# Kernel tuning notes

Hardware: AMD Instinct MI355X
Metric: run time of the kernel (lower is better)

The kernel has to match this reference:

```python
import jax, jax.numpy as jnp
import numpy as np

D = 1024

def setup_inputs() -> dict:
    key = jax.random.key(0)
    ks = jax.random.split(key, 9)
    s = 1.0 / np.sqrt(D)
    x = jax.random.normal(ks[0], (8, 4096, D), dtype=jnp.float32)
    Wq = jax.random.uniform(ks[1], (D, D), jnp.float32, -s, s)
    bq = jax.random.uniform(ks[2], (D,), jnp.float32, -s, s)
    Wk = jax.random.uniform(ks[3], (D, D), jnp.float32, -s, s)
    bk = jax.random.uniform(ks[4], (D,), jnp.float32, -s, s)
    Wv = jax.random.uniform(ks[5], (D, D), jnp.float32, -s, s)
    bv = jax.random.uniform(ks[6], (D,), jnp.float32, -s, s)
    Wo = jax.random.uniform(ks[7], (D, D), jnp.float32, -s, s)
    bo = jax.random.uniform(ks[8], (D,), jnp.float32, -s, s)
    return {"x": x, "Wq": Wq, "bq": bq, "Wk": Wk, "bk": bk,
            "Wv": Wv, "bv": bv, "Wo": Wo, "bo": bo}

def reference(x, Wq, bq, Wk, bk, Wv, bv, Wo, bo):
    # Linear projections (torch Linear: x @ W.T + b)
    Q = x @ Wq.T + bq
    K = x @ Wk.T + bk
    V = x @ Wv.T + bv
    # elu+1 feature map (positive features)
    Q = jax.nn.elu(Q) + 1.0
    K = jax.nn.elu(K) + 1.0
    # KV outer-product accumulation over sequence: [b, d, e]
    KV = jnp.einsum('bnd,bne->bde', K, V)
    # normalizer Z: [b, n]
    Z = jnp.einsum('bnd,bd->bn', Q, K.sum(axis=1) + 1e-6)
    context = jnp.einsum('bnd,bde->bne', Q, KV) / Z[..., None]
    return context @ Wo.T + bo
```

## Files before the change

### kernel.cpp

```cpp
#include <hip/hip_runtime.h>
#include <stdint.h>

typedef unsigned short u16;
typedef __attribute__((ext_vector_type(8))) short short8;
typedef __attribute__((ext_vector_type(4))) float f32x4;

#define SEQ    4096
#define NB     8
#define DMODEL 1024
#define MTOT   (NB*SEQ)

static __device__ __forceinline__ float bf2f(u16 u){
  union { float f; uint32_t i; } v; v.i = ((uint32_t)u) << 16; return v.f;
}
static __device__ __forceinline__ u16 f2bf(float f){
  union { float f; uint32_t i; } v; v.f = f;
  uint32_t i = v.i + 0x7FFFu + ((v.i >> 16) & 1u);
  return (u16)(i >> 16);
}

static __device__ __forceinline__ void stage16(const void* g, void* l){
  __builtin_amdgcn_global_load_lds(
      (const __attribute__((address_space(1))) void*)g,
      (__attribute__((address_space(3))) void*)l,
      16, 0, 0);
}

__global__ void cvt_f32_bf16(const float* __restrict__ s, u16* __restrict__ d, int n){
  int i = (blockIdx.x * 256 + threadIdx.x) * 8;
  if (i >= n) return;
  float4 a = *(const float4*)(s + i);
  float4 b = *(const float4*)(s + i + 4);
  union { u16 h[8]; short8 v; } o;
  o.h[0]=f2bf(a.x); o.h[1]=f2bf(a.y); o.h[2]=f2bf(a.z); o.h[3]=f2bf(a.w);
  o.h[4]=f2bf(b.x); o.h[5]=f2bf(b.y); o.h[6]=f2bf(b.z); o.h[7]=f2bf(b.w);
  *(short8*)(d + i) = o.v;
}

__global__ __launch_bounds__(256)
void cvt_tr(const float* __restrict__ in, u16* __restrict__ outN,
            u16* __restrict__ outT, int R, int C)
{
  __shared__ float t[64][65];
  const int tid = threadIdx.x;
  const int ntc = C >> 6;
  const int tr = blockIdx.x / ntc, tc = blockIdx.x % ntc;
  const int r0 = tr << 6, c0 = tc << 6;
  const int lrow = tid >> 4, lc4 = (tid & 15) << 2;
  #pragma unroll
  for (int p = 0; p < 4; p++){
    float4 v = *(const float4*)(in + (size_t)(r0 + p*16 + lrow) * C + c0 + lc4);
    t[p*16 + lrow][lc4+0] = v.x; t[p*16 + lrow][lc4+1] = v.y;
    t[p*16 + lrow][lc4+2] = v.z; t[p*16 + lrow][lc4+3] = v.w;
  }
  __syncthreads();
  const int wrow = tid >> 3, wc8 = (tid & 7) << 3;
  if (outN){
    #pragma unroll
    for (int p = 0; p < 2; p++){
      int r = p*32 + wrow;
      union { u16 h[8]; short8 v; } o;
      #pragma unroll
      for (int j = 0; j < 8; j++) o.h[j] = f2bf(t[r][wc8 + j]);
      *(short8*)(outN + (size_t)(r0 + r) * C + c0 + wc8) = o.v;
    }
  }
  #pragma unroll
  for (int p = 0; p < 2; p++){
    int c = p*32 + wrow;
    union { u16 h[8]; short8 v; } o;
    #pragma unroll
    for (int j = 0; j < 8; j++) o.h[j] = f2bf(t[wc8 + j][c]);
    *(short8*)(outT + (size_t)(c0 + c) * R + r0 + wc8) = o.v;
  }
}

__global__ void bo2_kernel(const float* __restrict__ Wo, const float* __restrict__ bv,
                           const float* __restrict__ bo, float* __restrict__ bo2){
  int o = blockIdx.x * 4 + (threadIdx.x >> 6);
  int lane = threadIdx.x & 63;
  const float* row = Wo + (size_t)o * DMODEL;
  float s = 0.f;
  #pragma unroll
  for (int j = 0; j < 4; j++){
    float4 w = *(const float4*)(row + j*256 + lane*4);
    float4 b = *(const float4*)(bv  + j*256 + lane*4);
    s += w.x*b.x + w.y*b.y + w.z*b.z + w.w*b.w;
  }
  for (int off = 32; off; off >>= 1) s += __shfl_xor(s, off);
  if (lane == 0) bo2[o] = bo[o] + s;
}

__global__ void ksum_kernel(const u16* __restrict__ Kt, float* __restrict__ Ksum){
  int wid  = blockIdx.x * 4 + (threadIdx.x >> 6);
  int lane = threadIdx.x & 63;
  int d = wid & 1023, b = wid >> 10;
  const u16* row = Kt + (size_t)d * MTOT + (size_t)b * SEQ;
  float s = 0.f;
  #pragma unroll
  for (int j = 0; j < 8; j++){
    short8 v = *(const short8*)(row + j * 512 + lane * 8);
    #pragma unroll
    for (int t = 0; t < 8; t++) s += bf2f((u16)v[t]);
  }
  for (int off = 32; off; off >>= 1) s += __shfl_xor(s, off);
  if (lane == 0) Ksum[wid] = s + 1e-6f;
}

__global__ void z_kernel(const u16* __restrict__ Qb, const float* __restrict__ Ksum,
                         float* __restrict__ Z){
  int n    = blockIdx.x * 4 + (threadIdx.x >> 6);
  int lane = threadIdx.x & 63;
  const u16*   qrow = Qb + (size_t)n * DMODEL;
  const float* ks   = Ksum + (size_t)(n >> 12) * DMODEL;
  float s = 0.f;
  #pragma unroll
  for (int j = 0; j < 2; j++){
    int base = j * 512 + lane * 8;
    short8 q  = *(const short8*)(qrow + base);
    float4 k0 = *(const float4*)(ks + base);
    float4 k1 = *(const float4*)(ks + base + 4);
    s += bf2f((u16)q[0])*k0.x + bf2f((u16)q[1])*k0.y + bf2f((u16)q[2])*k0.z + bf2f((u16)q[3])*k0.w
       + bf2f((u16)q[4])*k1.x + bf2f((u16)q[5])*k1.y + bf2f((u16)q[6])*k1.z + bf2f((u16)q[7])*k1.w;
  }
  for (int off = 32; off; off >>= 1) s += __shfl_xor(s, off);
  if (lane == 0) Z[n] = s;
}

__global__ __launch_bounds__(256)
void gemm_bt(const u16* __restrict__ A, int ldA,
             const u16* __restrict__ BT, int ldBT, int Kdim,
             u16* __restrict__ Obf, int ldO)
{
  __shared__ u16 Al[128 * 32];
  __shared__ u16 Bl[128 * 32];
  const int tid  = threadIdx.x;
  const int lane = tid & 63;
  const int w    = tid >> 6;
  const int tcol = blockIdx.x;
  const int trow = blockIdx.y;

  const u16* Ap = A  + (size_t)trow * 128 * ldA;
  const u16* Bp = BT + (size_t)tcol * 128 * ldBT;

  f32x4 acc[4][4] = {};
  const int srow = (lane >> 2);
  const int scol = (lane & 3) * 8;

  for (int k0 = 0; k0 < Kdim; k0 += 32){
    #pragma unroll
    for (int i = 0; i < 2; i++){
      int r = w * 32 + i * 16 + srow;
      stage16(Ap + (size_t)r * ldA  + k0 + scol, (char*)Al + w * 2048 + i * 1024);
      stage16(Bp + (size_t)r * ldBT + k0 + scol, (char*)Bl + w * 2048 + i * 1024);
    }
    __syncthreads();
    const int mr = (w >> 1) * 64, nc = (w & 1) * 64;
    const int lr = lane & 15, lk = (lane >> 4) * 8;
    short8 av[4], bv[4];
    #pragma unroll
    for (int mi = 0; mi < 4; mi++) av[mi] = *(const short8*)&Al[(mr + mi*16 + lr)*32 + lk];
    #pragma unroll
    for (int nj = 0; nj < 4; nj++) bv[nj] = *(const short8*)&Bl[(nc + nj*16 + lr)*32 + lk];
    #pragma unroll
    for (int mi = 0; mi < 4; mi++)
      #pragma unroll
      for (int nj = 0; nj < 4; nj++)
        acc[mi][nj] = __builtin_amdgcn_mfma_f32_16x16x32_bf16(av[mi], bv[nj], acc[mi][nj], 0, 0, 0);
    __syncthreads();
  }

  const int mr = (w >> 1) * 64, nc = (w & 1) * 64;
  const int lr = lane & 15, lq = lane >> 4;
  #pragma unroll
  for (int mi = 0; mi < 4; mi++)
    #pragma unroll
    for (int r = 0; r < 4; r++){
      const size_t grow = (size_t)trow * 128 + mr + mi * 16 + lq * 4 + r;
      #pragma unroll
      for (int nj = 0; nj < 4; nj++){
        const size_t gcol = (size_t)tcol * 128 + nc + nj * 16 + lr;
        Obf[grow * ldO + gcol] = f2bf(acc[mi][nj][r]);
      }
    }
}

static __device__ __forceinline__ void stage_chunk(
    const u16* __restrict__ g, int ld, int k0, u16* smem, int baseU16, int tid){
  #pragma unroll
  for (int c = 0; c < 2; c++){
    int lin = c * 512 + tid;
    int row = lin >> 3;
    int slotL = (lin & 7) ^ (row & 7);
    stage16(g + (size_t)row * ld + k0 + slotL * 8,
            (char*)smem + baseU16 * 2 + (c * 8 + (tid >> 6)) * 1024);
  }
}

template<int EPI>
__global__ __launch_bounds__(512, 2)
void gemm8(const u16* __restrict__ A, int ldA,
           const u16* __restrict__ BT, int ldBT, int NT,
           const float* __restrict__ bias, const float* __restrict__ Zv,
           u16* __restrict__ Obf, float* __restrict__ Of32, int ldO)
{
  __shared__ u16 smem[65536];
  const int tid  = threadIdx.x;
  const int lane = tid & 63;
  const int w    = tid >> 6;
  const int wm   = w >> 2, wn = w & 3;
  const int lr   = lane & 15, kq = lane >> 4;

  const int nwg  = gridDim.x;
  const int orig = blockIdx.x;
  const int work = (orig & 7) * (nwg >> 3) + (orig >> 3);
  int trow, tcol; size_t aoff = 0, boff = 0, ooff = 0;
  if (EPI == 1)      { trow = work & 3; tcol = work >> 2; }
  else if (EPI == 3) { int zb = work >> 4, sub = work & 15;
                       trow = sub & 3; tcol = sub >> 2;
                       aoff = (size_t)zb * SEQ; boff = aoff; ooff = (size_t)zb << 20; }
  else if (EPI == 4) { int zb = work >> 4, sub = work & 15;
                       trow = sub & 3; tcol = sub >> 2;
                       boff = (size_t)zb << 20; ooff = (size_t)zb << 20; }
  else               { tcol = work & 3; trow = work >> 2;
                       if (EPI == 2) boff = (size_t)(trow >> 4) << 20; }
  const int tileM = trow * 256, tileN = tcol * 256;

  const u16* Ag = A  + aoff + (size_t)tileM * ldA;
  const u16* Bg = BT + boff + (size_t)tileN * ldBT;

  f32x4 acc[8][4] = {};

#define STAGE(buf, k0) do { \
    stage_chunk(Ag,                    ldA,  (k0), smem, (buf) + 0,     tid); \
    stage_chunk(Ag + (size_t)128*ldA,  ldA,  (k0), smem, (buf) + 8192,  tid); \
    stage_chunk(Bg,                    ldBT, (k0), smem, (buf) + 16384, tid); \
    stage_chunk(Bg + (size_t)128*ldBT, ldBT, (k0), smem, (buf) + 24576, tid); \
  } while(0)

#define LDSA(MF, KC) (*(const short8*)(smem + cb + (wm*128 + (MF)*16 + lr)*64 + ((((KC)*4 + kq) ^ (lr & 7)) * 8)))
#define LDSB(NF, KC) (*(const short8*)(smem + cb + 16384 + (wn*64 + (NF)*16 + lr)*64 + ((((KC)*4 + kq) ^ (lr & 7)) * 8)))

  STAGE(0, 0);
  STAGE(32768, 64);
  asm volatile("s_waitcnt vmcnt(8)" ::: "memory");
  __builtin_amdgcn_sched_barrier(0);
  __builtin_amdgcn_s_barrier();

  for (int t = 0; t < NT; t++){
    const int cb = (t & 1) << 15;
    short8 af[4][2], ah[4][2], bf[4][2];
    #pragma unroll
    for (int i = 0; i < 4; i++){ af[i][0] = LDSA(i, 0);   af[i][1] = LDSA(i, 1); }
    #pragma unroll
    for (int i = 0; i < 4; i++){ bf[i][0] = LDSB(i, 0);   bf[i][1] = LDSB(i, 1); }
    __builtin_amdgcn_s_setprio(1);
    #pragma unroll
    for (int mi = 0; mi < 4; mi++)
      #pragma unroll
      for (int nj = 0; nj < 4; nj++)
        #pragma unroll
        for (int kc = 0; kc < 2; kc++)
          acc[mi][nj] = __builtin_amdgcn_mfma_f32_16x16x32_bf16(
              af[mi][kc], bf[nj][kc], acc[mi][nj], 0, 0, 0);
    __builtin_amdgcn_s_setprio(0);
    #pragma unroll
    for (int i = 0; i < 4; i++){ ah[i][0] = LDSA(4+i, 0); ah[i][1] = LDSA(4+i, 1); }
    __builtin_amdgcn_s_setprio(1);
    #pragma unroll
    for (int mi = 0; mi < 4; mi++)
      #pragma unroll
      for (int nj = 0; nj < 4; nj++)
        #pragma unroll
        for (int kc = 0; kc < 2; kc++)
          acc[4+mi][nj] = __builtin_amdgcn_mfma_f32_16x16x32_bf16(
              ah[mi][kc], bf[nj][kc], acc[4+mi][nj], 0, 0, 0);
    __builtin_amdgcn_s_setprio(0);

    __builtin_amdgcn_sched_barrier(0);
    __builtin_amdgcn_s_barrier();
    const int kNN = (t + 2 < NT ? t + 2 : NT - 1) * 64;
    STAGE(cb, kNN);
    asm volatile("s_waitcnt vmcnt(8)" ::: "memory");
    __builtin_amdgcn_sched_barrier(0);
    __builtin_amdgcn_s_barrier();
  }

#undef STAGE
#undef LDSA
#undef LDSB

  #pragma unroll
  for (int mf = 0; mf < 8; mf++){
    #pragma unroll
    for (int r = 0; r < 4; r++){
      const int grow = tileM + wm*128 + mf*16 + kq*4 + r;
      float rowB = 0.f, zin = 0.f;
      if (EPI == 1) rowB = bias[grow];
      if (EPI == 2) zin = 1.f / Zv[grow];
      #pragma unroll
      for (int nf = 0; nf < 4; nf++){
        const int gcol = tileN + wn*64 + nf*16 + lr;
        float v = acc[mf][nf][r];
        if (EPI == 0) { v += bias[gcol]; v = (v > 0.f) ? v + 1.f : __expf(v); }
        if (EPI == 1) { v += rowB;       v = (v > 0.f) ? v + 1.f : __expf(v); }
        if constexpr (EPI == 2) Of32[(size_t)grow * ldO + gcol] = v * zin + bias[gcol];
        else                    Obf [ooff + (size_t)grow * ldO + gcol] = f2bf(v);
      }
    }
  }
}

extern "C" void kernel_launch(void* const* d_in, const int* in_sizes, int n_in,
                              void* d_out, int out_size, void* d_ws, size_t ws_size,
                              hipStream_t stream)
{
  const float* x  = (const float*)d_in[0];
  const float* Wq = (const float*)d_in[1];
  const float* bq = (const float*)d_in[2];
  const float* Wk = (const float*)d_in[3];
  const float* bk = (const float*)d_in[4];
  const float* Wv = (const float*)d_in[5];
  const float* bv = (const float*)d_in[6];
  const float* Wo = (const float*)d_in[7];
  const float* bo = (const float*)d_in[8];
  float* out = (float*)d_out;

  char* ws = (char*)d_ws;
  u16*   xb  = (u16*)(ws + 0);
  u16*   Tt  = (u16*)(ws + 0);
  u16*   Gt  = (u16*)(ws + 16777216);
  u16*   xT  = (u16*)(ws + 67108864);
  u16*   Qb  = (u16*)(ws + 134217728);
  u16*   Kt  = (u16*)(ws + 201326592);
  u16*   Wqb = (u16*)(ws + 268435456);
  u16*   Wkb = (u16*)(ws + 270532608);
  u16*   Wob = (u16*)(ws + 272629760);
  u16*   WvT = (u16*)(ws + 274726912);
  u16*   W2b = (u16*)(ws + 276824064);
  float* Ks  = (float*)(ws + 278921216);
  float* Zp  = (float*)(ws + 278953984);
  float* bo2 = (float*)(ws + 279085056);

  cvt_tr<<<8192, 256, 0, stream>>>(x, xb, xT, MTOT, DMODEL);
  cvt_f32_bf16<<<512, 256, 0, stream>>>(Wq, Wqb, DMODEL * DMODEL);
  cvt_f32_bf16<<<512, 256, 0, stream>>>(Wk, Wkb, DMODEL * DMODEL);
  cvt_f32_bf16<<<512, 256, 0, stream>>>(Wo, Wob, DMODEL * DMODEL);
  cvt_tr<<<256, 256, 0, stream>>>(Wv, (u16*)nullptr, WvT, DMODEL, DMODEL);
  bo2_kernel<<<256, 256, 0, stream>>>(Wo, bv, bo, bo2);

  gemm8<0><<<512, 512, 0, stream>>>(xb, 1024, Wqb, 1024, 16, bq, nullptr,
                                    Qb, nullptr, 1024);
  gemm8<1><<<512, 512, 0, stream>>>(Wkb, 1024, xb, 1024, 16, bk, nullptr,
                                    Kt, nullptr, MTOT);
  ksum_kernel<<<2048, 256, 0, stream>>>(Kt, Ks);
  z_kernel<<<8192, 256, 0, stream>>>(Qb, Ks, Zp);
  gemm8<3><<<128, 512, 0, stream>>>(Kt, MTOT, xT, MTOT, 64, nullptr, nullptr,
                                    Tt, nullptr, 1024);
  gemm_bt<<<dim3(8, 8, 1), dim3(256), 0, stream>>>(Wob, 1024, WvT, 1024, 1024,
                                                   W2b, 1024);
  gemm8<4><<<128, 512, 0, stream>>>(W2b, 1024, Tt, 1024, 16, nullptr, nullptr,
                                    Gt, nullptr, 1024);
  gemm8<2><<<512, 512, 0, stream>>>(Qb, 1024, Gt, 1024, 16, bo2, Zp,
                                    nullptr, out, 1024);
}
```

Measured before the change: 492.2 us.

## Use half-height 128x256 GEMM tiles for the per-batch KV and W2 stages

Adds a gemm8h variant with 128x256 tiles, smaller LDS and fewer accumulators, and uses it for the per-batch K^T·x and W2·T GEMMs. Those launches grow from 128 to 256 workgroups so more CUs get work. The W2·T stage now runs as a single GEMM over all batches with a concatenated Gt layout (ld 8192) instead of per-batch offsets, and the final GEMM indexes Gt accordingly. The W2b precompute is moved earlier in the stream. Smaller tiles lower arithmetic intensity per workgroup in exchange for better CU fill.

Measured after the change: 441.0 us, median of 4. 1.12x faster.

```diff
diff --git a/kernel.cpp b/kernel.cpp
--- a/kernel.cpp
+++ b/kernel.cpp
@@ -214,19 +214,13 @@
   const int nwg  = gridDim.x;
   const int orig = blockIdx.x;
   const int work = (orig & 7) * (nwg >> 3) + (orig >> 3);
-  int trow, tcol; size_t aoff = 0, boff = 0, ooff = 0;
+  int trow, tcol; size_t boff = 0;
   if (EPI == 1)      { trow = work & 3; tcol = work >> 2; }
-  else if (EPI == 3) { int zb = work >> 4, sub = work & 15;
-                       trow = sub & 3; tcol = sub >> 2;
-                       aoff = (size_t)zb * SEQ; boff = aoff; ooff = (size_t)zb << 20; }
-  else if (EPI == 4) { int zb = work >> 4, sub = work & 15;
-                       trow = sub & 3; tcol = sub >> 2;
-                       boff = (size_t)zb << 20; ooff = (size_t)zb << 20; }
   else               { tcol = work & 3; trow = work >> 2;
-                       if (EPI == 2) boff = (size_t)(trow >> 4) << 20; }
+                       if (EPI == 2) boff = (size_t)(trow >> 4) * 1024; }
   const int tileM = trow * 256, tileN = tcol * 256;
 
-  const u16* Ag = A  + aoff + (size_t)tileM * ldA;
+  const u16* Ag = A + (size_t)tileM * ldA;
   const u16* Bg = BT + boff + (size_t)tileN * ldBT;
 
   f32x4 acc[8][4] = {};
@@ -305,7 +299,92 @@
         if (EPI == 0) { v += bias[gcol]; v = (v > 0.f) ? v + 1.f : __expf(v); }
         if (EPI == 1) { v += rowB;       v = (v > 0.f) ? v + 1.f : __expf(v); }
         if constexpr (EPI == 2) Of32[(size_t)grow * ldO + gcol] = v * zin + bias[gcol];
-        else                    Obf [ooff + (size_t)grow * ldO + gcol] = f2bf(v);
+        else                    Obf [(size_t)grow * ldO + gcol] = f2bf(v);
+      }
+    }
+  }
+}
+
+template<int EPI>
+__global__ __launch_bounds__(512, 2)
+void gemm8h(const u16* __restrict__ A, int ldA,
+            const u16* __restrict__ BT, int ldBT, int NT,
+            u16* __restrict__ Obf, int ldO)
+{
+  __shared__ u16 smem[49152];
+  const int tid  = threadIdx.x;
+  const int lane = tid & 63;
+  const int w    = tid >> 6;
+  const int wm   = w >> 2, wn = w & 3;
+  const int lr   = lane & 15, kq = lane >> 4;
+
+  const int orig = blockIdx.x;
+  const int work = (orig & 7) * 32 + (orig >> 3);
+  int trow, tcol; size_t aoff = 0, boff = 0, ooff = 0;
+  if (EPI == 3) { int zb = work >> 5, sub = work & 31;
+                  trow = sub & 7; tcol = sub >> 3;
+                  aoff = (size_t)zb * SEQ; boff = aoff; ooff = (size_t)zb << 20; }
+  else          { trow = work & 7; tcol = work >> 3; }
+  const int tileM = trow * 128, tileN = tcol * 256;
+
+  const u16* Ag = A  + aoff + (size_t)tileM * ldA;
+  const u16* Bg = BT + boff + (size_t)tileN * ldBT;
+
+  f32x4 acc[4][4] = {};
+
+#define STAGEH(buf, k0) do { \
+    stage_chunk(Ag,                    ldA,  (k0), smem, (buf) + 0,     tid); \
+    stage_chunk(Bg,                    ldBT, (k0), smem, (buf) + 8192,  tid); \
+    stage_chunk(Bg + (size_t)128*ldBT, ldBT, (k0), smem, (buf) + 16384, tid); \
+  } while(0)
+
+#define LDSAH(MF, KC) (*(const short8*)(smem + cb + (wm*64 + (MF)*16 + lr)*64 + ((((KC)*4 + kq) ^ (lr & 7)) * 8)))
+#define LDSBH(NF, KC) (*(const short8*)(smem + cb + 8192 + (wn*64 + (NF)*16 + lr)*64 + ((((KC)*4 + kq) ^ (lr & 7)) * 8)))
+
+  STAGEH(0, 0);
+  STAGEH(24576, 64);
+  asm volatile("s_waitcnt vmcnt(6)" ::: "memory");
+  __builtin_amdgcn_sched_barrier(0);
+  __builtin_amdgcn_s_barrier();
+
+  for (int t = 0; t < NT; t++){
+    const int cb = (t & 1) * 24576;
+    short8 af[4][2], bf[4][2];
+    #pragma unroll
+    for (int i = 0; i < 4; i++){ af[i][0] = LDSAH(i, 0); af[i][1] = LDSAH(i, 1); }
+    #pragma unroll
+    for (int i = 0; i < 4; i++){ bf[i][0] = LDSBH(i, 0); bf[i][1] = LDSBH(i, 1); }
+    __builtin_amdgcn_s_setprio(1);
+    #pragma unroll
+    for (int mi = 0; mi < 4; mi++)
+      #pragma unroll
+      for (int nj = 0; nj < 4; nj++)
+        #pragma unroll
+        for (int kc = 0; kc < 2; kc++)
+          acc[mi][nj] = __builtin_amdgcn_mfma_f32_16x16x32_bf16(
+              af[mi][kc], bf[nj][kc], acc[mi][nj], 0, 0, 0);
+    __builtin_amdgcn_s_setprio(0);
+    __builtin_amdgcn_sched_barrier(0);
+    __builtin_amdgcn_s_barrier();
+    const int kNN = (t + 2 < NT ? t + 2 : NT - 1) * 64;
+    STAGEH(cb, kNN);
+    asm volatile("s_waitcnt vmcnt(6)" ::: "memory");
+    __builtin_amdgcn_sched_barrier(0);
+    __builtin_amdgcn_s_barrier();
+  }
+#undef STAGEH
+#undef LDSAH
+#undef LDSBH
+
+  #pragma unroll
+  for (int mf = 0; mf < 4; mf++){
+    #pragma unroll
+    for (int r = 0; r < 4; r++){
+      const int grow = tileM + wm*64 + mf*16 + kq*4 + r;
+      #pragma unroll
+      for (int nf = 0; nf < 4; nf++){
+        const int gcol = tileN + wn*64 + nf*16 + lr;
+        Obf[ooff + (size_t)grow * ldO + gcol] = f2bf(acc[mf][nf][r]);
       }
     }
   }
@@ -348,6 +427,8 @@
   cvt_f32_bf16<<<512, 256, 0, stream>>>(Wo, Wob, DMODEL * DMODEL);
   cvt_tr<<<256, 256, 0, stream>>>(Wv, (u16*)nullptr, WvT, DMODEL, DMODEL);
   bo2_kernel<<<256, 256, 0, stream>>>(Wo, bv, bo, bo2);
+  gemm_bt<<<dim3(8, 8, 1), dim3(256), 0, stream>>>(Wob, 1024, WvT, 1024, 1024,
+                                                   W2b, 1024);
 
   gemm8<0><<<512, 512, 0, stream>>>(xb, 1024, Wqb, 1024, 16, bq, nullptr,
                                     Qb, nullptr, 1024);
@@ -355,12 +436,8 @@
                                     Kt, nullptr, MTOT);
   ksum_kernel<<<2048, 256, 0, stream>>>(Kt, Ks);
   z_kernel<<<8192, 256, 0, stream>>>(Qb, Ks, Zp);
-  gemm8<3><<<128, 512, 0, stream>>>(Kt, MTOT, xT, MTOT, 64, nullptr, nullptr,
-                                    Tt, nullptr, 1024);
-  gemm_bt<<<dim3(8, 8, 1), dim3(256), 0, stream>>>(Wob, 1024, WvT, 1024, 1024,
-                                                   W2b, 1024);
-  gemm8<4><<<128, 512, 0, stream>>>(W2b, 1024, Tt, 1024, 16, nullptr, nullptr,
-                                    Gt, nullptr, 1024);
-  gemm8<2><<<512, 512, 0, stream>>>(Qb, 1024, Gt, 1024, 16, bo2, Zp,
+  gemm8h<3><<<256, 512, 0, stream>>>(Kt, MTOT, xT, MTOT, 64, Tt, 1024);
+  gemm8h<4><<<256, 512, 0, stream>>>(W2b, 1024, Tt, 1024, 16, Gt, 8192);
+  gemm8<2><<<512, 512, 0, stream>>>(Qb, 1024, Gt, 8192, 16, bo2, Zp,
                                     nullptr, out, 1024);
 }
```
